# Optimization experiments

Hardware: AMD Instinct MI355X
Metric: run time of the kernel (lower is better)

The kernel has to match this reference:

```python
import jax, jax.numpy as jnp
import numpy as np

B = 65536
X_DIM = 32
H_DIM = 128


def setup_inputs() -> dict:
    key = jax.random.key(0)
    ks = jax.random.split(key, 11)
    f_scale = 0.1
    x = jax.random.uniform(ks[0], (B, X_DIM), dtype=jnp.float32)
    z = jax.random.normal(ks[1], (B, X_DIM), dtype=jnp.float32)
    # M: rand*0.2 with zero diagonal (use_mask=True, empty dag_seed)
    M = jax.random.uniform(ks[2], (X_DIM, X_DIM), dtype=jnp.float32) * 0.2
    M = M * (1.0 - jnp.eye(X_DIM, dtype=jnp.float32))
    # per-node input linears fc_i: weight [h, x_dim+1], column i zeroed (1e-16)
    Wi = jax.random.normal(ks[3], (X_DIM, H_DIM, X_DIM + 1), dtype=jnp.float32) * f_scale * 0.1
    col_mask = 1.0 - jnp.eye(X_DIM + 1, dtype=jnp.float32)[:X_DIM]  # [x_dim, x_dim+1]
    Wi = Wi * col_mask[:, None, :] + 1e-16 * (1.0 - col_mask)[:, None, :]
    bi = jax.random.normal(ks[4], (X_DIM, H_DIM), dtype=jnp.float32) * 0.01
    wf = jax.random.normal(ks[5], (X_DIM, H_DIM), dtype=jnp.float32) * f_scale * 0.1
    bf = jax.random.normal(ks[6], (X_DIM,), dtype=jnp.float32) * 0.01
    W1 = jax.random.normal(ks[7], (H_DIM, H_DIM), dtype=jnp.float32) * f_scale * 0.1
    b1 = jax.random.normal(ks[8], (H_DIM,), dtype=jnp.float32) * 0.01
    W2 = jax.random.normal(ks[9], (H_DIM, H_DIM), dtype=jnp.float32) * f_scale * 0.1
    b2 = jax.random.normal(ks[10], (H_DIM,), dtype=jnp.float32) * 0.01
    return {"x": x, "z": z, "M": M, "Wi": Wi, "bi": bi, "wf": wf,
            "bf": bf, "W1": W1, "b1": b1, "W2": W2, "b2": b2}


def reference(x, z, M, Wi, bi, wf, bf, W1, b1, W2, b2):
    x_dim = M.shape[0]
    eye = jnp.eye(x_dim, dtype=x.dtype)

    def step(out, xs):
        m_col, oh, Wi_i, bi_i, wf_i, bf_i, z_i = xs
        # x_masked = out * M[:, i]; x_masked[:, i] = 0
        xm = out * (m_col * (1.0 - oh))                       # [B, x_dim]
        # fc_i: cat([x_masked, z_i]) @ W.T + b, then ReLU
        h = jax.nn.relu(xm @ Wi_i[:, :x_dim].T
                        + z_i[:, None] * Wi_i[:, x_dim]
                        + bi_i)                                # [B, h]
        # shared 2-layer MLP
        h = jax.nn.relu(h @ W1.T + b1)
        h = jax.nn.relu(h @ W2.T + b2)
        val = jax.nn.sigmoid(h @ wf_i + bf_i)                  # [B]
        out = out * (1.0 - oh) + val[:, None] * oh             # out[:, i] = val
        return out, None

    xs = (M.T, eye, Wi, bi, wf, bf, z.T)
    out, _ = jax.lax.scan(step, x, xs)
    return out
```

## Files before the change

### kernel.cpp

```cpp
#include <hip/hip_runtime.h>
#include <math.h>

#define XD 32
#define HD 128

typedef float f32x16 __attribute__((ext_vector_type(16)));
typedef int v2i __attribute__((ext_vector_type(2)));
typedef int i32x8 __attribute__((ext_vector_type(8)));

#if __has_builtin(__builtin_amdgcn_cvt_pk_fp8_f32)
#define HAVE_CVT_FP8 1
#endif

static __device__ __forceinline__ unsigned char f2e4m3(float f){
  if (!(f==f)) return 0x7F;
  unsigned u = __float_as_uint(f);
  unsigned s = (u>>24)&0x80;
  float a = fabsf(f);
  if (a >= 464.f) return (unsigned char)(s|0x7E);
  if (a < 0.0009765625f) return (unsigned char)s;
  int e = (int)((u>>23)&0xFF) - 127;
  if (e < -6){
    int m = (int)rintf(ldexpf(a, 9));
    if (m >= 8) return (unsigned char)(s|0x08);
    return (unsigned char)(s|(unsigned)m);
  }
  int m = (int)rintf(ldexpf(a, 3-e));
  if (m == 16){ ++e; m = 8; }
  if (e > 8) return (unsigned char)(s|0x7E);
  return (unsigned char)(s | (unsigned)((e+7)<<3) | (unsigned)(m-8));
}

template<bool HI>
static __device__ __forceinline__ int cvtpk_fp8(float a, float b, int old){
#ifdef HAVE_CVT_FP8
  return __builtin_amdgcn_cvt_pk_fp8_f32(a, b, old, HI);
#else
  int w = (int)f2e4m3(a) | ((int)f2e4m3(b) << 8);
  return HI ? ((old & 0x0000FFFF) | (w << 16)) : ((old & (int)0xFFFF0000) | w);
#endif
}

static __device__ __forceinline__ void plswap(int &x, int &y){
#if __has_builtin(__builtin_amdgcn_permlane32_swap)
  v2i r = __builtin_amdgcn_permlane32_swap(x, y, false, false);
  x = r[0]; y = r[1];
#else
  unsigned lane = threadIdx.x & 63u;
  int sx = __shfl_xor(x, 32, 64);
  int sy = __shfl_xor(y, 32, 64);
  int nx = (lane < 32) ? x : sy;
  int ny = (lane < 32) ? sx : y;
  x = nx; y = ny;
#endif
}

static __device__ __forceinline__ i32x8 c2mx(const f32x16 &ca, const f32x16 &cb){
  i32x8 fr;
#pragma unroll
  for (int q = 0; q < 4; ++q){
    int x = cvtpk_fp8<false>(fmaxf(ca[q*4+0],0.f), fmaxf(ca[q*4+1],0.f), 0);
    x     = cvtpk_fp8<true >(fmaxf(ca[q*4+2],0.f), fmaxf(ca[q*4+3],0.f), x);
    int y = cvtpk_fp8<false>(fmaxf(cb[q*4+0],0.f), fmaxf(cb[q*4+1],0.f), 0);
    y     = cvtpk_fp8<true >(fmaxf(cb[q*4+2],0.f), fmaxf(cb[q*4+3],0.f), y);
    plswap(x, y);
    fr[q*2]   = x;
    fr[q*2+1] = y;
  }
  return fr;
}

static __device__ __forceinline__ f32x16 mfma_mx(i32x8 a, i32x8 b, f32x16 c){
  return __builtin_amdgcn_mfma_scale_f32_32x32x64_f8f6f4(
           a, b, c, 0, 0, 0, 0x7F7F7F7F, 0, 0x7F7F7F7F);
}

static __device__ __forceinline__ void ld8(const float* __restrict__ p, float* dst){
  float4 a = *(const float4*)p, b = *(const float4*)(p+4);
  dst[0]=a.x; dst[1]=a.y; dst[2]=a.z; dst[3]=a.w;
  dst[4]=b.x; dst[5]=b.y; dst[6]=b.z; dst[7]=b.w;
}

static __device__ __forceinline__ f32x16 load_bias16(const float* __restrict__ p, int half){
  f32x16 bv;
#pragma unroll
  for (int rg=0; rg<4; ++rg){
    const float4 t = *(const float4*)(p + rg*8 + half*4);
    bv[rg*4+0]=t.x; bv[rg*4+1]=t.y; bv[rg*4+2]=t.z; bv[rg*4+3]=t.w;
  }
  return bv;
}

__global__ void prep(const float* __restrict__ Wi, const float* __restrict__ bi,
                     const float* __restrict__ W1, const float* __restrict__ b1,
                     const float* __restrict__ W2, const float* __restrict__ b2,
                     const float* __restrict__ M,  const float* __restrict__ wf,
                     unsigned char* __restrict__ wip, unsigned char* __restrict__ w1p,
                     unsigned char* __restrict__ w2p, unsigned char* __restrict__ wfp,
                     float* __restrict__ Mt, float* __restrict__ bi8,
                     float* __restrict__ b1s, float* __restrict__ b2s){
  int b = (int)blockIdx.x;
  int l = (int)threadIdx.x;
  int h = l >> 5, cl = l & 31;
  if (b < 256){
    int i = b >> 3, kt = (b >> 2) & 1, fo = b & 3;
    int row = fo*32 + cl;
    unsigned char bytes[8];
#pragma unroll
    for (int j = 0; j < 8; ++j){
      int k = kt*16 + h*8 + j;
      int src = (k == i) ? XD : k;
      bytes[j] = f2e4m3(8.f * Wi[((size_t)i*HD + row)*(XD+1) + src]);
    }
    long v8; __builtin_memcpy(&v8, bytes, 8);
    *(long*)(wip + ((size_t)b*64 + l)*8) = v8;
  } else if (b < 272){
    const float* W = (b < 264) ? W1 : W2;
    unsigned char* dp = (b < 264) ? w1p : w2p;
    int f = (b - 256) & 7;
    int fo = f >> 1, f2 = f & 1;
    int row = fo*32 + cl;
    union { unsigned char bt[32]; int4 v[2]; } u;
#pragma unroll
    for (int j = 0; j < 32; ++j)
      u.bt[j] = f2e4m3(8.f * W[(size_t)row*HD + f2*64 + h*32 + j]);
    *(int4*)(dp + ((size_t)((f*2+0)*64 + l))*16) = u.v[0];
    *(int4*)(dp + ((size_t)((f*2+1)*64 + l))*16) = u.v[1];
  } else if (b < 336){
    int f = b - 272;
    int i = f >> 1, f2 = f & 1;
    union { unsigned char bt[32]; int4 v[2]; } u;
#pragma unroll
    for (int j = 0; j < 32; ++j){
      float v = (cl == 0) ? 64.f * wf[(size_t)i*HD + f2*64 + h*32 + j] : 0.f;
      u.bt[j] = f2e4m3(v);
    }
    *(int4*)(wfp + ((size_t)f*64 + l)*32)      = u.v[0];
    *(int4*)(wfp + ((size_t)f*64 + l)*32 + 16) = u.v[1];
  } else if (b == 336){
#pragma unroll
    for (int t = 0; t < 16; ++t){
      int idx = t*64 + l;
      int i = idx >> 5, k = idx & 31;
      Mt[i*32 + k] = M[k*32 + i];
    }
  } else {
    for (int t = 0; t < 64; ++t){
      int idx = t*64 + l;
      bi8[idx] = 8.f * bi[idx];
    }
#pragma unroll
    for (int t = 0; t < 2; ++t){
      b1s[t*64 + l] = 64.f  * b1[t*64 + l];
      b2s[t*64 + l] = 512.f * b2[t*64 + l];
    }
  }
}

static __device__ __forceinline__ void pack_xb(const float (&st)[16], const float (&mtv)[16],
                                               float zvv, int i, bool hm, long (&xb)[2]){
  int xbi[2][2];
#pragma unroll
  for (int kt = 0; kt < 2; ++kt)
#pragma unroll
    for (int d = 0; d < 2; ++d){
      float v0 = st[kt*8+4*d+0]*mtv[kt*8+4*d+0];
      float v1 = st[kt*8+4*d+1]*mtv[kt*8+4*d+1];
      float v2 = st[kt*8+4*d+2]*mtv[kt*8+4*d+2];
      float v3 = st[kt*8+4*d+3]*mtv[kt*8+4*d+3];
      int w = cvtpk_fp8<false>(v0, v1, 0);
      xbi[kt][d] = cvtpk_fp8<true>(v2, v3, w);
    }
  const int kti = i>>4, di = (i>>2)&1, sh = 8*(i&3);
  const int msk = ~(0xFF << sh);
  int pz = cvtpk_fp8<false>(zvv, 0.f, 0) & 0xFF;
  int ins = pz << sh;
#pragma unroll
  for (int kt = 0; kt < 2; ++kt)
#pragma unroll
    for (int d = 0; d < 2; ++d)
      if (kt == kti && d == di){
        int mod = (xbi[kt][d] & msk) | ins;
        xbi[kt][d] = hm ? mod : xbi[kt][d];
      }
#pragma unroll
  for (int kt = 0; kt < 2; ++kt)
    xb[kt] = (long)(((unsigned long)(unsigned)xbi[kt][0]) |
                    ((unsigned long)(unsigned)xbi[kt][1] << 32));
}

static __device__ __forceinline__ i32x8 ld_mx(const unsigned char* __restrict__ p){
  union { int4 h[2]; i32x8 v; } u;
  u.h[0] = *(const int4*)(p);
  u.h[1] = *(const int4*)(p + 16);
  return u.v;
}

static __device__ __forceinline__ i32x8 ld_mx_lds(const int4* base, int f, int lane){
  union { int4 h[2]; i32x8 v; } u;
  u.h[0] = base[(f*2+0)*64 + lane];
  u.h[1] = base[(f*2+1)*64 + lane];
  return u.v;
}

__global__ void __launch_bounds__(256, 1)
genkern(const float* __restrict__ x, const float* __restrict__ z,
        const float* __restrict__ bf,
        const unsigned char* __restrict__ wip, const unsigned char* __restrict__ w1p,
        const unsigned char* __restrict__ w2p, const unsigned char* __restrict__ wfp,
        const float* __restrict__ Mt, const float* __restrict__ bi8,
        const float* __restrict__ b1s, const float* __restrict__ b2s,
        float* __restrict__ out)
{
  __shared__ int4 wlds[2048];

  const int tid  = (int)threadIdx.x;
  const int lane = tid & 63;
  const int wv   = tid >> 6;
  const int half = lane >> 5, col = lane & 31;
  const long rbase = (long)blockIdx.x * 256 + wv * 64;

  {
    const int4* s1 = (const int4*)w1p;
    const int4* s2 = (const int4*)w2p;
#pragma unroll
    for (int t = 0; t < 4; ++t)
      wlds[t*256 + tid] = s1[t*256 + tid];
#pragma unroll
    for (int t = 0; t < 4; ++t)
      wlds[1024 + t*256 + tid] = s2[t*256 + tid];
  }

  float stA[16], stB[16];
#pragma unroll
  for (int kt = 0; kt < 2; ++kt){
    ld8(x + (rbase + col)*XD + kt*16 + half*8,      &stA[kt*8]);
    ld8(x + (rbase + 32 + col)*XD + kt*16 + half*8, &stB[kt*8]);
  }

  __syncthreads();

  long wif[2][4];
  i32x8 wfx[2];
  float zA, zB;
#pragma unroll
  for (int kt = 0; kt < 2; ++kt)
#pragma unroll
    for (int fo = 0; fo < 4; ++fo)
      wif[kt][fo] = *(const long*)(wip + (((size_t)(kt*4 + fo))*64 + lane)*8);
  wfx[0] = ld_mx(wfp + ((size_t)0*64 + lane)*32);
  wfx[1] = ld_mx(wfp + ((size_t)1*64 + lane)*32);
  zA = z[(rbase + col)*XD + 0];
  zB = z[(rbase + 32 + col)*XD + 0];

#pragma unroll 1
  for (int i = 0; i < XD; ++i){
    const int ip = (i + 1) & (XD - 1);
    const bool hm = (half == ((i>>3)&1));
    const int slot_i = ((i>>4)<<3) | (i&7);
    const float bfv = bf[i];

    float mtv[16];
#pragma unroll
    for (int kt = 0; kt < 2; ++kt)
      ld8(Mt + i*32 + kt*16 + half*8, &mtv[kt*8]);

    long xbA[2], xbB[2];
    pack_xb(stA, mtv, zA, i, hm, xbA);
    pack_xb(stB, mtv, zB, i, hm, xbB);
    zA = z[(rbase + col)*XD + ip];
    zB = z[(rbase + 32 + col)*XD + ip];

    f32x16 accA[4], accB[4];
#pragma unroll
    for (int fo = 0; fo < 4; ++fo){
      f32x16 bc = load_bias16(bi8 + (size_t)i*HD + fo*32, half);
      accA[fo] = __builtin_amdgcn_mfma_f32_32x32x16_fp8_fp8(wif[0][fo], xbA[0], bc, 0,0,0);
      accB[fo] = __builtin_amdgcn_mfma_f32_32x32x16_fp8_fp8(wif[0][fo], xbB[0], bc, 0,0,0);
    }
#pragma unroll
    for (int fo = 0; fo < 4; ++fo){
      accA[fo] = __builtin_amdgcn_mfma_f32_32x32x16_fp8_fp8(wif[1][fo], xbA[1], accA[fo], 0,0,0);
      accB[fo] = __builtin_amdgcn_mfma_f32_32x32x16_fp8_fp8(wif[1][fo], xbB[1], accB[fo], 0,0,0);
    }
#pragma unroll
    for (int kt = 0; kt < 2; ++kt)
#pragma unroll
      for (int fo = 0; fo < 4; ++fo)
        wif[kt][fo] = *(const long*)(wip + (((size_t)(ip*8 + kt*4 + fo))*64 + lane)*8);

    {
      i32x8 mxA0 = c2mx(accA[0], accA[1]);
      i32x8 mxA1 = c2mx(accA[2], accA[3]);
      i32x8 mxB0 = c2mx(accB[0], accB[1]);
      i32x8 mxB1 = c2mx(accB[2], accB[3]);
#pragma unroll
      for (int fo = 0; fo < 4; ++fo){
        i32x8 w = ld_mx_lds(wlds, fo*2+0, lane);
        f32x16 bc = load_bias16(b1s + fo*32, half);
        accA[fo] = mfma_mx(w, mxA0, bc);
        accB[fo] = mfma_mx(w, mxB0, bc);
      }
#pragma unroll
      for (int fo = 0; fo < 4; ++fo){
        i32x8 w = ld_mx_lds(wlds, fo*2+1, lane);
        accA[fo] = mfma_mx(w, mxA1, accA[fo]);
        accB[fo] = mfma_mx(w, mxB1, accB[fo]);
      }
    }

    {
      i32x8 mxA0 = c2mx(accA[0], accA[1]);
      i32x8 mxA1 = c2mx(accA[2], accA[3]);
      i32x8 mxB0 = c2mx(accB[0], accB[1]);
      i32x8 mxB1 = c2mx(accB[2], accB[3]);
#pragma unroll
      for (int fo = 0; fo < 4; ++fo){
        i32x8 w = ld_mx_lds(wlds, 8 + fo*2+0, lane);
        f32x16 bc = load_bias16(b2s + fo*32, half);
        accA[fo] = mfma_mx(w, mxA0, bc);
        accB[fo] = mfma_mx(w, mxB0, bc);
      }
#pragma unroll
      for (int fo = 0; fo < 4; ++fo){
        i32x8 w = ld_mx_lds(wlds, 8 + fo*2+1, lane);
        accA[fo] = mfma_mx(w, mxA1, accA[fo]);
        accB[fo] = mfma_mx(w, mxB1, accB[fo]);
      }
    }

    {
      i32x8 mxA0 = c2mx(accA[0], accA[1]);
      i32x8 mxA1 = c2mx(accA[2], accA[3]);
      i32x8 mxB0 = c2mx(accB[0], accB[1]);
      i32x8 mxB1 = c2mx(accB[2], accB[3]);
      f32x16 eA, eB;
#pragma unroll
      for (int q = 0; q < 16; ++q){ eA[q] = 0.f; eB[q] = 0.f; }
      eA = mfma_mx(wfx[0], mxA0, eA);
      eB = mfma_mx(wfx[0], mxB0, eB);
      eA = mfma_mx(wfx[1], mxA1, eA);
      eB = mfma_mx(wfx[1], mxB1, eB);
      float uA = eA[0], uB = eB[0];
      float sA = __shfl_xor(uA, 32, 64);
      float sB = __shfl_xor(uB, 32, 64);
      float tA = half ? sA : uA;
      float tB = half ? sB : uB;
      float vA = 1.f/(1.f + __expf(-(tA*(1.f/32768.f) + bfv)));
      float vB = 1.f/(1.f + __expf(-(tB*(1.f/32768.f) + bfv)));
#pragma unroll
      for (int s = 0; s < 16; ++s)
        if (s == slot_i){
          stA[s] = hm ? vA : stA[s];
          stB[s] = hm ? vB : stB[s];
        }
    }
    wfx[0] = ld_mx(wfp + ((size_t)(ip*2 + 0)*64 + lane)*32);
    wfx[1] = ld_mx(wfp + ((size_t)(ip*2 + 1)*64 + lane)*32);
  }

#pragma unroll
  for (int kt = 0; kt < 2; ++kt){
    float* pA = out + (rbase + col)*XD + kt*16 + half*8;
    float* pB = out + (rbase + 32 + col)*XD + kt*16 + half*8;
    float4 a, b;
    a.x = stA[kt*8+0]; a.y = stA[kt*8+1]; a.z = stA[kt*8+2]; a.w = stA[kt*8+3];
    b.x = stA[kt*8+4]; b.y = stA[kt*8+5]; b.z = stA[kt*8+6]; b.w = stA[kt*8+7];
    *(float4*)pA = a; *(float4*)(pA+4) = b;
    a.x = stB[kt*8+0]; a.y = stB[kt*8+1]; a.z = stB[kt*8+2]; a.w = stB[kt*8+3];
    b.x = stB[kt*8+4]; b.y = stB[kt*8+5]; b.z = stB[kt*8+6]; b.w = stB[kt*8+7];
    *(float4*)pB = a; *(float4*)(pB+4) = b;
  }
}

extern "C" void kernel_launch(void* const* d_in, const int* in_sizes, int n_in,
                              void* d_out, int out_size, void* d_ws, size_t ws_size,
                              hipStream_t stream){
  (void)in_sizes; (void)n_in; (void)out_size; (void)ws_size;
  const float* x  = (const float*)d_in[0];
  const float* z  = (const float*)d_in[1];
  const float* M  = (const float*)d_in[2];
  const float* Wi = (const float*)d_in[3];
  const float* bi = (const float*)d_in[4];
  const float* wf = (const float*)d_in[5];
  const float* bf = (const float*)d_in[6];
  const float* W1 = (const float*)d_in[7];
  const float* b1 = (const float*)d_in[8];
  const float* W2 = (const float*)d_in[9];
  const float* b2 = (const float*)d_in[10];

  unsigned char* wip = (unsigned char*)d_ws;
  unsigned char* w1p = wip + 131072;
  unsigned char* w2p = w1p + 16384;
  unsigned char* wfp = w2p + 16384;
  float*         Mt  = (float*)(wfp + 131072);
  float*         bi8 = Mt + 1024;
  float*         b1s = bi8 + 4096;
  float*         b2s = b1s + 128;

  prep<<<dim3(338), dim3(64), 0, stream>>>(Wi, bi, W1, b1, W2, b2, M, wf,
                                           wip, w1p, w2p, wfp, Mt, bi8, b1s, b2s);
  genkern<<<dim3(256), dim3(256), 0, stream>>>(x, z, bf, wip, w1p, w2p, wfp, Mt,
                                               bi8, b1s, b2s, (float*)d_out);
}
```

Measured before the change: 169.3 us.

## Process one 32-row tile per wave and double grid with two waves per SIMD

Each wave now handles a single 32-row tile instead of two interleaved tiles (A/B), halving per-wave work and register pressure, and the grid doubles to 512 blocks so all rows stay covered. The launch attribute changes from one wave per EU to amdgpu_waves_per_eu(2,2), aiming for more resident waves so that MFMA latency and the serial per-step dependency chain are hidden by thread-level parallelism rather than by interleaving two independent tiles within one wave. The trade-off is that each wave loses the instruction-level overlap from the two independent chains and weights are reloaded by twice as many waves, while the register budget is halved.

```diff
diff --git a/kernel.cpp b/kernel.cpp
--- a/kernel.cpp
+++ b/kernel.cpp
@@ -203,7 +203,7 @@
   return u.v;
 }
 
-__global__ void __launch_bounds__(256, 1)
+__global__ void __launch_bounds__(256) __attribute__((amdgpu_waves_per_eu(2, 2)))
 genkern(const float* __restrict__ x, const float* __restrict__ z,
         const float* __restrict__ bf,
         const unsigned char* __restrict__ wip, const unsigned char* __restrict__ w1p,
@@ -218,7 +218,7 @@
   const int lane = tid & 63;
   const int wv   = tid >> 6;
   const int half = lane >> 5, col = lane & 31;
-  const long rbase = (long)blockIdx.x * 256 + wv * 64;
+  const long rbase = (long)blockIdx.x * 128 + wv * 32;
 
   {
     const int4* s1 = (const int4*)w1p;
@@ -231,18 +231,16 @@
       wlds[1024 + t*256 + tid] = s2[t*256 + tid];
   }
 
-  float stA[16], stB[16];
-#pragma unroll
-  for (int kt = 0; kt < 2; ++kt){
-    ld8(x + (rbase + col)*XD + kt*16 + half*8,      &stA[kt*8]);
-    ld8(x + (rbase + 32 + col)*XD + kt*16 + half*8, &stB[kt*8]);
-  }
+  float st[16];
+#pragma unroll
+  for (int kt = 0; kt < 2; ++kt)
+    ld8(x + (rbase + col)*XD + kt*16 + half*8, &st[kt*8]);
 
   __syncthreads();
 
   long wif[2][4];
   i32x8 wfx[2];
-  float zA, zB;
+  float zA;
 #pragma unroll
   for (int kt = 0; kt < 2; ++kt)
 #pragma unroll
@@ -251,7 +249,6 @@
   wfx[0] = ld_mx(wfp + ((size_t)0*64 + lane)*32);
   wfx[1] = ld_mx(wfp + ((size_t)1*64 + lane)*32);
   zA = z[(rbase + col)*XD + 0];
-  zB = z[(rbase + 32 + col)*XD + 0];
 
 #pragma unroll 1
   for (int i = 0; i < XD; ++i){
@@ -265,24 +262,19 @@
     for (int kt = 0; kt < 2; ++kt)
       ld8(Mt + i*32 + kt*16 + half*8, &mtv[kt*8]);
 
-    long xbA[2], xbB[2];
-    pack_xb(stA, mtv, zA, i, hm, xbA);
-    pack_xb(stB, mtv, zB, i, hm, xbB);
+    long xb[2];
+    pack_xb(st, mtv, zA, i, hm, xb);
     zA = z[(rbase + col)*XD + ip];
-    zB = z[(rbase + 32 + col)*XD + ip];
-
-    f32x16 accA[4], accB[4];
+
+    f32x16 acc[4];
 #pragma unroll
     for (int fo = 0; fo < 4; ++fo){
       f32x16 bc = load_bias16(bi8 + (size_t)i*HD + fo*32, half);
-      accA[fo] = __builtin_amdgcn_mfma_f32_32x32x16_fp8_fp8(wif[0][fo], xbA[0], bc, 0,0,0);
-      accB[fo] = __builtin_amdgcn_mfma_f32_32x32x16_fp8_fp8(wif[0][fo], xbB[0], bc, 0,0,0);
-    }
-#pragma unroll
-    for (int fo = 0; fo < 4; ++fo){
-      accA[fo] = __builtin_amdgcn_mfma_f32_32x32x16_fp8_fp8(wif[1][fo], xbA[1], accA[fo], 0,0,0);
-      accB[fo] = __builtin_amdgcn_mfma_f32_32x32x16_fp8_fp8(wif[1][fo], xbB[1], accB[fo], 0,0,0);
-    }
+      acc[fo] = __builtin_amdgcn_mfma_f32_32x32x16_fp8_fp8(wif[0][fo], xb[0], bc, 0,0,0);
+    }
+#pragma unroll
+    for (int fo = 0; fo < 4; ++fo)
+      acc[fo] = __builtin_amdgcn_mfma_f32_32x32x16_fp8_fp8(wif[1][fo], xb[1], acc[fo], 0,0,0);
 #pragma unroll
     for (int kt = 0; kt < 2; ++kt)
 #pragma unroll
@@ -290,70 +282,53 @@
         wif[kt][fo] = *(const long*)(wip + (((size_t)(ip*8 + kt*4 + fo))*64 + lane)*8);
 
     {
-      i32x8 mxA0 = c2mx(accA[0], accA[1]);
-      i32x8 mxA1 = c2mx(accA[2], accA[3]);
-      i32x8 mxB0 = c2mx(accB[0], accB[1]);
-      i32x8 mxB1 = c2mx(accB[2], accB[3]);
+      i32x8 mx0 = c2mx(acc[0], acc[1]);
+      i32x8 mx1 = c2mx(acc[2], acc[3]);
 #pragma unroll
       for (int fo = 0; fo < 4; ++fo){
         i32x8 w = ld_mx_lds(wlds, fo*2+0, lane);
         f32x16 bc = load_bias16(b1s + fo*32, half);
-        accA[fo] = mfma_mx(w, mxA0, bc);
-        accB[fo] = mfma_mx(w, mxB0, bc);
+        acc[fo] = mfma_mx(w, mx0, bc);
       }
 #pragma unroll
       for (int fo = 0; fo < 4; ++fo){
         i32x8 w = ld_mx_lds(wlds, fo*2+1, lane);
-        accA[fo] = mfma_mx(w, mxA1, accA[fo]);
-        accB[fo] = mfma_mx(w, mxB1, accB[fo]);
+        acc[fo] = mfma_mx(w, mx1, acc[fo]);
       }
     }
 
     {
-      i32x8 mxA0 = c2mx(accA[0], accA[1]);
-      i32x8 mxA1 = c2mx(accA[2], accA[3]);
-      i32x8 mxB0 = c2mx(accB[0], accB[1]);
-      i32x8 mxB1 = c2mx(accB[2], accB[3]);
+      i32x8 mx0 = c2mx(acc[0], acc[1]);
+      i32x8 mx1 = c2mx(acc[2], acc[3]);
 #pragma unroll
       for (int fo = 0; fo < 4; ++fo){
         i32x8 w = ld_mx_lds(wlds, 8 + fo*2+0, lane);
         f32x16 bc = load_bias16(b2s + fo*32, half);
-        accA[fo] = mfma_mx(w, mxA0, bc);
-        accB[fo] = mfma_mx(w, mxB0, bc);
+        acc[fo] = mfma_mx(w, mx0, bc);
       }
 #pragma unroll
       for (int fo = 0; fo < 4; ++fo){
         i32x8 w = ld_mx_lds(wlds, 8 + fo*2+1, lane);
-        accA[fo] = mfma_mx(w, mxA1, accA[fo]);
-        accB[fo] = mfma_mx(w, mxB1, accB[fo]);
+        acc[fo] = mfma_mx(w, mx1, acc[fo]);
       }
     }
 
     {
-      i32x8 mxA0 = c2mx(accA[0], accA[1]);
-      i32x8 mxA1 = c2mx(accA[2], accA[3]);
-      i32x8 mxB0 = c2mx(accB[0], accB[1]);
-      i32x8 mxB1 = c2mx(accB[2], accB[3]);
-      f32x16 eA, eB;
-#pragma unroll
-      for (int q = 0; q < 16; ++q){ eA[q] = 0.f; eB[q] = 0.f; }
-      eA = mfma_mx(wfx[0], mxA0, eA);
-      eB = mfma_mx(wfx[0], mxB0, eB);
-      eA = mfma_mx(wfx[1], mxA1, eA);
-      eB = mfma_mx(wfx[1], mxB1, eB);
-      float uA = eA[0], uB = eB[0];
-      float sA = __shfl_xor(uA, 32, 64);
-      float sB = __shfl_xor(uB, 32, 64);
-      float tA = half ? sA : uA;
-      float tB = half ? sB : uB;
-      float vA = 1.f/(1.f + __expf(-(tA*(1.f/32768.f) + bfv)));
-      float vB = 1.f/(1.f + __expf(-(tB*(1.f/32768.f) + bfv)));
-#pragma unroll
-      for (int s = 0; s < 16; ++s)
-        if (s == slot_i){
-          stA[s] = hm ? vA : stA[s];
-          stB[s] = hm ? vB : stB[s];
-        }
+      i32x8 mx0 = c2mx(acc[0], acc[1]);
+      i32x8 mx1 = c2mx(acc[2], acc[3]);
+      f32x16 e;
+#pragma unroll
+      for (int q = 0; q < 16; ++q) e[q] = 0.f;
+      e = mfma_mx(wfx[0], mx0, e);
+      e = mfma_mx(wfx[1], mx1, e);
+      float u = e[0];
+      float s = __shfl_xor(u, 32, 64);
+      float t = half ? s : u;
+      float v = 1.f/(1.f + __expf(-(t*(1.f/32768.f) + bfv)));
+#pragma unroll
+      for (int q = 0; q < 16; ++q)
+        if (q == slot_i)
+          st[q] = hm ? v : st[q];
     }
     wfx[0] = ld_mx(wfp + ((size_t)(ip*2 + 0)*64 + lane)*32);
     wfx[1] = ld_mx(wfp + ((size_t)(ip*2 + 1)*64 + lane)*32);
@@ -361,15 +336,12 @@
 
 #pragma unroll
   for (int kt = 0; kt < 2; ++kt){
-    float* pA = out + (rbase + col)*XD + kt*16 + half*8;
-    float* pB = out + (rbase + 32 + col)*XD + kt*16 + half*8;
+    float* p = out + (rbase + col)*XD + kt*16 + half*8;
     float4 a, b;
-    a.x = stA[kt*8+0]; a.y = stA[kt*8+1]; a.z = stA[kt*8+2]; a.w = stA[kt*8+3];
-    b.x = stA[kt*8+4]; b.y = stA[kt*8+5]; b.z = stA[kt*8+6]; b.w = stA[kt*8+7];
-    *(float4*)pA = a; *(float4*)(pA+4) = b;
-    a.x = stB[kt*8+0]; a.y = stB[kt*8+1]; a.z = stB[kt*8+2]; a.w = stB[kt*8+3];
-    b.x = stB[kt*8+4]; b.y = stB[kt*8+5]; b.z = stB[kt*8+6]; b.w = stB[kt*8+7];
-    *(float4*)pB = a; *(float4*)(pB+4) = b;
+    a.x = st[kt*8+0]; a.y = st[kt*8+1]; a.z = st[kt*8+2]; a.w = st[kt*8+3];
+    b.x = st[kt*8+4]; b.y = st[kt*8+5]; b.z = st[kt*8+6]; b.w = st[kt*8+7];
+    *(float4*)p = a;
+    *(float4*)(p+4) = b;
   }
 }
 
@@ -400,6 +372,6 @@
 
   prep<<<dim3(338), dim3(64), 0, stream>>>(Wi, bi, W1, b1, W2, b2, M, wf,
                                            wip, w1p, w2p, wfp, Mt, bi8, b1s, b2s);
-  genkern<<<dim3(256), dim3(256), 0, stream>>>(x, z, bf, wip, w1p, w2p, wfp, Mt,
+  genkern<<<dim3(512), dim3(256), 0, stream>>>(x, z, bf, wip, w1p, w2p, wfp, Mt,
                                                bi8, b1s, b2s, (float*)d_out);
 }
```

New measurement: 397.7 us. 2.35x slower.
